# Kernel optimization log

Measured on AMD Instinct MI355X. Metric: run time of the kernel, lower is better.

The kernel has to match this reference:

```python
import jax, jax.numpy as jnp
import numpy as np

B, S, D = 2, 2048, 1024
H = 16
HD = D // H  # 64
SCALE = 1.0 / np.sqrt(HD).astype(np.float32)


def setup_inputs() -> dict:
    key = jax.random.key(0)
    ks = jax.random.split(key, 5)
    std = 0.02
    return {
        "x": jax.random.normal(ks[0], (B, S, D), dtype=jnp.float32),
        "W_qkv": jax.random.normal(ks[1], (D, 3 * D), dtype=jnp.float32) * std,
        "b_qkv": jnp.zeros((3 * D,), dtype=jnp.float32),
        "W_proj": jax.random.normal(ks[2], (D, D), dtype=jnp.float32) * std,
        "b_proj": jnp.zeros((D,), dtype=jnp.float32),
    }


def reference(x, W_qkv, b_qkv, W_proj, b_proj):
    bsz, seq_len, _ = x.shape
    qkv = x @ W_qkv + b_qkv  # [B,S,3D]
    qkv = qkv.reshape(bsz, seq_len, 3, H, HD)
    qkv = jnp.transpose(qkv, (2, 0, 3, 1, 4))  # [3,B,H,S,HD]
    q, k, v = qkv[0], qkv[1], qkv[2]
    scores = jnp.einsum("bhqd,bhkd->bhqk", q, k) * SCALE  # [B,H,S,S]
    causal = jnp.tril(jnp.ones((seq_len, seq_len), dtype=bool))
    scores = jnp.where(causal[None, None], scores, -jnp.inf)
    weights = jax.nn.softmax(scores, axis=-1)
    attn = jnp.einsum("bhqk,bhkd->bhqd", weights, v)  # [B,H,S,HD]
    attn = jnp.transpose(attn, (0, 2, 1, 3)).reshape(bsz, seq_len, H * HD)
    return attn @ W_proj + b_proj
```

## Files before the change

### kernel.cpp

```cpp
#include <hip/hip_runtime.h>
#include <stdint.h>

#define NB 2
#define NS 2048
#define ND 1024
#define NH 16
#define NHD 64
#define SCALE_QL2 0.1803368801111244f

typedef __attribute__((ext_vector_type(8))) short bf16x8;
typedef __attribute__((ext_vector_type(4))) float f32x4;
typedef __attribute__((ext_vector_type(16))) float f32x16;
typedef __attribute__((ext_vector_type(8))) unsigned short u16x8;

__device__ __forceinline__ unsigned short f2bf(float f) {
  union { float f; unsigned u; } v; v.f = f;
  unsigned r = v.u + 0x7FFFu + ((v.u >> 16) & 1u);
  return (unsigned short)(r >> 16);
}

__device__ __forceinline__ float bf2f(unsigned short u) {
  union { unsigned u; float f; } v; v.u = ((unsigned)u) << 16;
  return v.f;
}

__device__ __forceinline__ float fexp2(float x) { return __builtin_amdgcn_exp2f(x); }

__device__ __forceinline__ unsigned cvtpk(float a, float b) {
  unsigned r;
  asm("v_cvt_pk_bf16_f32 %0, %1, %2" : "=v"(r) : "v"(a), "v"(b));
  return r;
}

__device__ __forceinline__ void plswap(unsigned& a, unsigned& b) {
  asm("v_permlane32_swap_b32 %0, %1" : "+v"(a), "+v"(b));
}

__device__ __forceinline__ void gload16(const void* g, void* l) {
  __builtin_amdgcn_global_load_lds(
      (const __attribute__((address_space(1))) unsigned int*)g,
      (__attribute__((address_space(3))) unsigned int*)l, 16, 0, 0);
}


__global__ void cvt_x(const float* __restrict__ in, unsigned short* __restrict__ out) {
  int i = blockIdx.x * 256 + threadIdx.x;
  const float4* p = (const float4*)in + (size_t)i * 2;
  float4 a = p[0], b = p[1];
  u16x8 o;
  o[0] = f2bf(a.x); o[1] = f2bf(a.y); o[2] = f2bf(a.z); o[3] = f2bf(a.w);
  o[4] = f2bf(b.x); o[5] = f2bf(b.y); o[6] = f2bf(b.z); o[7] = f2bf(b.w);
  *((u16x8*)out + i) = o;
}

__global__ void transpose_cvt(const float* __restrict__ W, unsigned short* __restrict__ WT,
                              int rows, int cols) {
  __shared__ float tile[32][33];
  int bc = blockIdx.x * 32;
  int br = blockIdx.y * 32;
  int tx = threadIdx.x & 31, ty = threadIdx.x >> 5;
#pragma unroll
  for (int i = 0; i < 4; ++i)
    tile[ty + i * 8][tx] = W[(size_t)(br + ty + i * 8) * cols + bc + tx];
  __syncthreads();
#pragma unroll
  for (int i = 0; i < 4; ++i)
    WT[(size_t)(bc + ty + i * 8) * rows + br + tx] = f2bf(tile[tx][ty + i * 8]);
}

template <int EPI, int BN, int MINW>
__global__ __launch_bounds__(256, MINW) void gemm_bt(
    const unsigned short* __restrict__ A, const unsigned short* __restrict__ Bt,
    const float* __restrict__ bias, int NT,
    unsigned short* __restrict__ Oq, unsigned short* __restrict__ Ok,
    unsigned short* __restrict__ Ov, float* __restrict__ Of) {
  constexpr int WN = BN / 2;
  constexpr int NI = BN / 32;
  constexpr int RB = BN / 32;
  __shared__ __align__(16) unsigned short lA[128 * 64];
  __shared__ __align__(16) unsigned short lB[BN * 64];

  int bid = blockIdx.x;
  int cpx = gridDim.x >> 3;
  int swz = (bid & 7) * cpx + (bid >> 3);
  int mt = swz / NT, nt = swz % NT;
  int m0 = mt * 128, n0 = nt * BN;

  int t = threadIdx.x, lane = t & 63, w = t >> 6;
  int wm = w >> 1, wn = w & 1;

  f32x4 acc[4][NI] = {};

  const char* gA = (const char*)(A + (size_t)m0 * 1024);
  const char* gB = (const char*)(Bt + (size_t)n0 * 1024);

  for (int kt = 0; kt < 16; ++kt) {
    __syncthreads();
#pragma unroll
    for (int r = 0; r < 4; ++r) {
      int L = r * 4096 + t * 16;
      int row = L >> 7, cb = L & 127;
      int scb = cb ^ ((row & 7) << 4);
      gload16(gA + (size_t)row * 2048 + kt * 128 + scb, (char*)lA + (L - lane * 16));
    }
#pragma unroll
    for (int r = 0; r < RB; ++r) {
      int L = r * 4096 + t * 16;
      int row = L >> 7, cb = L & 127;
      int scb = cb ^ ((row & 7) << 4);
      gload16(gB + (size_t)row * 2048 + kt * 128 + scb, (char*)lB + (L - lane * 16));
    }
    __syncthreads();
#pragma unroll
    for (int kk = 0; kk < 2; ++kk) {
      bf16x8 af[4], bg[NI];
#pragma unroll
      for (int mi = 0; mi < 4; ++mi) {
        int row = wm * 64 + mi * 16 + (lane & 15);
        int byte = row * 128 + ((kk * 64 + (lane >> 4) * 16) ^ ((row & 7) << 4));
        af[mi] = *(const bf16x8*)((const char*)lA + byte);
      }
#pragma unroll
      for (int ni = 0; ni < NI; ++ni) {
        int row = wn * WN + ni * 16 + (lane & 15);
        int byte = row * 128 + ((kk * 64 + (lane >> 4) * 16) ^ ((row & 7) << 4));
        bg[ni] = *(const bf16x8*)((const char*)lB + byte);
      }
      __builtin_amdgcn_s_setprio(1);
#pragma unroll
      for (int mi = 0; mi < 4; ++mi)
#pragma unroll
        for (int ni = 0; ni < NI; ++ni)
          acc[mi][ni] = __builtin_amdgcn_mfma_f32_16x16x32_bf16(af[mi], bg[ni], acc[mi][ni], 0, 0, 0);
      __builtin_amdgcn_s_setprio(0);
    }
  }

#pragma unroll
  for (int mi = 0; mi < 4; ++mi)
#pragma unroll
    for (int ni = 0; ni < NI; ++ni) {
      int col = n0 + wn * WN + ni * 16 + (lane & 15);
      float bv = bias[col];
#pragma unroll
      for (int r = 0; r < 4; ++r) {
        int row = m0 + wm * 64 + mi * 16 + (lane >> 4) * 4 + r;
        float v = acc[mi][ni][r] + bv;
        if (EPI == 0) {
          int which = col >> 10, dd = col & 1023;
          int h = dd >> 6, hd = dd & 63;
          int b = row >> 11, s = row & 2047;
          size_t bh = (size_t)(b * 16 + h);
          if (which == 0)      Oq[(bh * 2048 + s) * 64 + hd] = f2bf(v * SCALE_QL2);
          else if (which == 1) Ok[(bh * 2048 + s) * 64 + hd] = f2bf(v);
          else                 Ov[(bh * 64 + hd) * 2048 + s] = f2bf(v);
        } else {
          Of[(size_t)row * 1024 + col] = v;
        }
      }
    }
}

__global__ __launch_bounds__(256, 4) void attn_split(
    const unsigned short* __restrict__ Qb, const unsigned short* __restrict__ Kb,
    const unsigned short* __restrict__ Vt,
    unsigned short* __restrict__ PO, float* __restrict__ PML) {
  __shared__ __align__(16) unsigned short lK[2][64 * 64];
  __shared__ __align__(16) unsigned short lV[2][64 * 64];

  int id = blockIdx.x;
  int bh = id & 31;
  int slot = 39 - (id >> 5);
  int a, g;
  if (slot < 4)       { a = 0; g = slot; }
  else if (slot < 12) { a = 1; g = slot - 4; }
  else if (slot < 24) { a = 2; g = slot - 12; }
  else                { a = 3; g = slot - 24; }
  int Tg = (a == 0) ? g : (a == 1) ? (g >> 1) : (a == 2) ? ((g * 11) >> 5) : (g >> 2);
  int T  = a * 4 + Tg;
  int c  = g - Tg * (a + 1);
  int t0 = c * 8;
  int tend = min(t0 + 7, 2 * T + 1);

  int t = threadIdx.x, lane = t & 63, w = t >> 6;
  int lo = lane & 31, hi = lane >> 5;
  int q0w = T * 128 + w * 32;
  int itmaxw = 2 * T + (w >> 1);
  int swzb = (lo & 7) << 4;

  const unsigned short* Qg = Qb + ((size_t)bh * 2048 + q0w + lo) * 64 + hi * 8;
  bf16x8 qf[4];
#pragma unroll
  for (int kk = 0; kk < 4; ++kk) qf[kk] = *(const bf16x8*)(Qg + kk * 16);

  f32x16 o0 = {}, o1 = {};
  float m = -1e30f, lsum = 0.f;

  const char* Kg = (const char*)(Kb + (size_t)bh * 2048 * 64);
  const char* Vg = (const char*)(Vt + (size_t)bh * 64 * 2048);

  int Lb = t * 16;
  auto STAGE = [&](int buf, int tile) {
    int s0 = tile * 64;
#pragma unroll
    for (int r = 0; r < 2; ++r) {
      int L = r * 4096 + Lb;
      int row = L >> 7, cb = L & 127;
      int scb = cb ^ ((row & 7) << 4);
      gload16(Kg + (size_t)(s0 + row) * 128 + scb, (char*)&lK[buf][0] + (L - lane * 16));
      gload16(Vg + (size_t)row * 4096 + (size_t)s0 * 2 + scb, (char*)&lV[buf][0] + (L - lane * 16));
    }
  };

  STAGE(0, t0);

  int cur = 0;
  for (int it = t0; it <= tend; ++it) {
    if (it < tend) {
      STAGE(cur ^ 1, it + 1);
      asm volatile("s_waitcnt vmcnt(4)" ::: "memory");
    } else {
      asm volatile("s_waitcnt vmcnt(0)" ::: "memory");
    }
    asm volatile("s_barrier" ::: "memory");

    if (it <= itmaxw) {
      const char* bK = (const char*)&lK[cur][0];
      const char* bV = (const char*)&lV[cur][0];

      f32x16 sv0 = {}, sv1 = {};
      __builtin_amdgcn_s_setprio(1);
#pragma unroll
      for (int kk = 0; kk < 4; ++kk) {
        int dby = 32 * kk + 16 * hi;
        bf16x8 k0 = *(const bf16x8*)(bK + lo * 128 + (dby ^ swzb));
        bf16x8 k1 = *(const bf16x8*)(bK + (32 + lo) * 128 + (dby ^ swzb));
        sv0 = __builtin_amdgcn_mfma_f32_32x32x16_bf16(k0, qf[kk], sv0, 0, 0, 0);
        sv1 = __builtin_amdgcn_mfma_f32_32x32x16_bf16(k1, qf[kk], sv1, 0, 0, 0);
      }
      __builtin_amdgcn_s_setprio(0);

      if (it == itmaxw) {
        int qg2 = q0w + lo, s0 = it * 64;
#pragma unroll
        for (int r = 0; r < 16; ++r) {
          int kv = s0 + (r & 3) + 8 * (r >> 2) + 4 * hi;
          if (kv > qg2) sv0[r] = -1e30f;
          if (kv + 32 > qg2) sv1[r] = -1e30f;
        }
      }

      float rmax = -1e30f;
#pragma unroll
      for (int r = 0; r < 16; ++r) rmax = fmaxf(rmax, fmaxf(sv0[r], sv1[r]));
      rmax = fmaxf(rmax, __shfl_xor(rmax, 32));

      if (__any(rmax > m + 8.0f)) {
        float mn = fmaxf(m, rmax);
        float sf = fexp2(m - mn);
        m = mn; lsum *= sf;
#pragma unroll
        for (int r = 0; r < 16; ++r) {
          float s = __shfl(sf, (r & 3) + 8 * (r >> 2) + 4 * hi);
          o0[r] *= s; o1[r] *= s;
        }
      }

      float rsum = 0.f;
#pragma unroll
      for (int r = 0; r < 16; ++r) {
        sv0[r] = fexp2(sv0[r] - m); rsum += sv0[r];
        sv1[r] = fexp2(sv1[r] - m); rsum += sv1[r];
      }
      rsum += __shfl_xor(rsum, 32);
      lsum += rsum;

      bf16x8 pa[4];
#pragma unroll
      for (int h2 = 0; h2 < 2; ++h2) {
        const f32x16& P = h2 ? sv1 : sv0;
#pragma unroll
        for (int kp = 0; kp < 2; ++kp) {
          unsigned a0 = cvtpk(P[8 * kp + 0], P[8 * kp + 1]);
          unsigned a1 = cvtpk(P[8 * kp + 2], P[8 * kp + 3]);
          unsigned b0 = cvtpk(P[8 * kp + 4], P[8 * kp + 5]);
          unsigned b1 = cvtpk(P[8 * kp + 6], P[8 * kp + 7]);
          plswap(a0, b0); plswap(a1, b1);
          union { unsigned u[4]; bf16x8 v; } uu;
          uu.u[0] = a0; uu.u[1] = a1; uu.u[2] = b0; uu.u[3] = b1;
          pa[2 * h2 + kp] = uu.v;
        }
      }

      __builtin_amdgcn_s_setprio(1);
#pragma unroll
      for (int dh = 0; dh < 2; ++dh) {
        f32x16& oc = dh ? o1 : o0;
#pragma unroll
        for (int ks = 0; ks < 4; ++ks) {
          int kvby = 32 * ks + 16 * hi;
          bf16x8 vf = *(const bf16x8*)(bV + (32 * dh + lo) * 128 + (kvby ^ swzb));
          oc = __builtin_amdgcn_mfma_f32_32x32x16_bf16(pa[ks], vf, oc, 0, 0, 0);
        }
      }
      __builtin_amdgcn_s_setprio(0);
    }

    asm volatile("s_barrier" ::: "memory");
    cur ^= 1;
  }

  size_t pobase = (size_t)(bh * 40 + slot) * 128;
#pragma unroll
  for (int r = 0; r < 16; ++r) {
    int crow = (r & 3) + 8 * (r >> 2) + 4 * hi;
    size_t rowoff = (pobase + w * 32 + crow) * 64 + lo;
    PO[rowoff]      = f2bf(o0[r]);
    PO[rowoff + 32] = f2bf(o1[r]);
  }
  if (hi == 0) {
    size_t mlbase = (size_t)(bh * 40 + slot) * 256 + w * 32 + lo;
    PML[mlbase]       = m;
    PML[mlbase + 128] = lsum;
  }
}

__global__ void attn_combine(const unsigned short* __restrict__ PO,
                             const float* __restrict__ PML,
                             unsigned short* __restrict__ attn) {
  int id = blockIdx.x * 256 + threadIdx.x;
  int dg = id & 7;
  int s  = (id >> 3) & 2047;
  int bh = id >> 14;
  int T = s >> 7, a = T >> 2;
  int nc = a + 1;
  int slot0 = (a + 1) * (T - 2 * a);
  int r128 = s & 127;
  int pb = bh * 40 + slot0;

  float mv[4], lv[4];
#pragma unroll
  for (int c = 0; c < 4; ++c) {
    if (c < nc) {
      mv[c] = PML[(size_t)(pb + c) * 256 + r128];
      lv[c] = PML[(size_t)(pb + c) * 256 + 128 + r128];
    } else { mv[c] = -1e30f; lv[c] = 0.f; }
  }
  float M = fmaxf(fmaxf(mv[0], mv[1]), fmaxf(mv[2], mv[3]));
  float wv[4], L = 0.f;
#pragma unroll
  for (int c = 0; c < 4; ++c) { wv[c] = fexp2(mv[c] - M); L += wv[c] * lv[c]; }
  float rcpL = 1.0f / L;

  float acc[8] = {};
#pragma unroll
  for (int c = 0; c < 4; ++c) {
    if (c < nc) {
      bf16x8 p = *(const bf16x8*)(PO + ((size_t)(pb + c) * 128 + r128) * 64 + dg * 8);
#pragma unroll
      for (int j = 0; j < 8; ++j) acc[j] += wv[c] * bf2f((unsigned short)p[j]);
    }
  }
  u16x8 o;
#pragma unroll
  for (int j = 0; j < 8; ++j) o[j] = f2bf(acc[j] * rcpL);
  int b = bh >> 4, h = bh & 15;
  *(u16x8*)(attn + ((size_t)(b * 2048 + s)) * 1024 + h * 64 + dg * 8) = o;
}

extern "C" void kernel_launch(void* const* d_in, const int* in_sizes, int n_in,
                              void* d_out, int out_size, void* d_ws, size_t ws_size,
                              hipStream_t stream) {
  const float* x      = (const float*)d_in[0];
  const float* W_qkv  = (const float*)d_in[1];
  const float* b_qkv  = (const float*)d_in[2];
  const float* W_proj = (const float*)d_in[3];
  const float* b_proj = (const float*)d_in[4];
  float* out = (float*)d_out;

  char* ws = (char*)d_ws;
  const size_t MB = 1u << 20;
  unsigned short* xb     = (unsigned short*)(ws);
  unsigned short* WqkvT  = (unsigned short*)(ws + 8 * MB);
  unsigned short* WprojT = (unsigned short*)(ws + 14 * MB);
  unsigned short* Qb     = (unsigned short*)(ws + 16 * MB);
  unsigned short* Kb     = (unsigned short*)(ws + 24 * MB);
  unsigned short* Vt     = (unsigned short*)(ws + 32 * MB);
  unsigned short* PO     = (unsigned short*)(ws + 40 * MB);
  float*          PML    = (float*)(ws + 60 * MB);
  unsigned short* attn   = xb;

  cvt_x<<<2048, 256, 0, stream>>>(x, xb);
  transpose_cvt<<<dim3(96, 32), 256, 0, stream>>>(W_qkv, WqkvT, 1024, 3072);
  transpose_cvt<<<dim3(32, 32), 256, 0, stream>>>(W_proj, WprojT, 1024, 1024);
  gemm_bt<0, 128, 2><<<768, 256, 0, stream>>>(xb, WqkvT, b_qkv, 24, Qb, Kb, Vt, nullptr);
  attn_split<<<1280, 256, 0, stream>>>(Qb, Kb, Vt, PO, PML);
  attn_combine<<<2048, 256, 0, stream>>>(PO, PML, attn);
  gemm_bt<1, 64, 5><<<512, 256, 0, stream>>>(attn, WprojT, b_proj, 16, nullptr, nullptr, nullptr, out);
}
```

Measured before the change: 121.1 us.

## Load K/V fragments directly from global memory, dropping LDS staging and barriers

Removes the double-buffered LDS staging of K and V tiles along with the block-wide barriers. Each wave now reads its MFMA operand fragments straight from global memory (relying on L1/L2 caching) and stops at its own causal limit. This eliminates LDS traffic and synchronization, but the four waves now fetch the same K/V data redundantly, and global-load latency is no longer hidden by prefetch.

```diff
diff --git a/kernel.cpp b/kernel.cpp
--- a/kernel.cpp
+++ b/kernel.cpp
@@ -165,9 +165,6 @@
     const unsigned short* __restrict__ Qb, const unsigned short* __restrict__ Kb,
     const unsigned short* __restrict__ Vt,
     unsigned short* __restrict__ PO, float* __restrict__ PML) {
-  __shared__ __align__(16) unsigned short lK[2][64 * 64];
-  __shared__ __align__(16) unsigned short lV[2][64 * 64];
-
   int id = blockIdx.x;
   int bh = id & 31;
   int slot = 39 - (id >> 5);
@@ -180,13 +177,12 @@
   int T  = a * 4 + Tg;
   int c  = g - Tg * (a + 1);
   int t0 = c * 8;
-  int tend = min(t0 + 7, 2 * T + 1);
 
   int t = threadIdx.x, lane = t & 63, w = t >> 6;
   int lo = lane & 31, hi = lane >> 5;
   int q0w = T * 128 + w * 32;
   int itmaxw = 2 * T + (w >> 1);
-  int swzb = (lo & 7) << 4;
+  int tendw = min(min(t0 + 7, 2 * T + 1), itmaxw);
 
   const unsigned short* Qg = Qb + ((size_t)bh * 2048 + q0w + lo) * 64 + hi * 8;
   bf16x8 qf[4];
@@ -196,118 +192,89 @@
   f32x16 o0 = {}, o1 = {};
   float m = -1e30f, lsum = 0.f;
 
-  const char* Kg = (const char*)(Kb + (size_t)bh * 2048 * 64);
-  const char* Vg = (const char*)(Vt + (size_t)bh * 64 * 2048);
-
-  int Lb = t * 16;
-  auto STAGE = [&](int buf, int tile) {
-    int s0 = tile * 64;
-#pragma unroll
-    for (int r = 0; r < 2; ++r) {
-      int L = r * 4096 + Lb;
-      int row = L >> 7, cb = L & 127;
-      int scb = cb ^ ((row & 7) << 4);
-      gload16(Kg + (size_t)(s0 + row) * 128 + scb, (char*)&lK[buf][0] + (L - lane * 16));
-      gload16(Vg + (size_t)row * 4096 + (size_t)s0 * 2 + scb, (char*)&lV[buf][0] + (L - lane * 16));
-    }
-  };
-
-  STAGE(0, t0);
-
-  int cur = 0;
-  for (int it = t0; it <= tend; ++it) {
-    if (it < tend) {
-      STAGE(cur ^ 1, it + 1);
-      asm volatile("s_waitcnt vmcnt(4)" ::: "memory");
-    } else {
-      asm volatile("s_waitcnt vmcnt(0)" ::: "memory");
-    }
-    asm volatile("s_barrier" ::: "memory");
-
-    if (it <= itmaxw) {
-      const char* bK = (const char*)&lK[cur][0];
-      const char* bV = (const char*)&lV[cur][0];
-
-      f32x16 sv0 = {}, sv1 = {};
-      __builtin_amdgcn_s_setprio(1);
-#pragma unroll
-      for (int kk = 0; kk < 4; ++kk) {
-        int dby = 32 * kk + 16 * hi;
-        bf16x8 k0 = *(const bf16x8*)(bK + lo * 128 + (dby ^ swzb));
-        bf16x8 k1 = *(const bf16x8*)(bK + (32 + lo) * 128 + (dby ^ swzb));
-        sv0 = __builtin_amdgcn_mfma_f32_32x32x16_bf16(k0, qf[kk], sv0, 0, 0, 0);
-        sv1 = __builtin_amdgcn_mfma_f32_32x32x16_bf16(k1, qf[kk], sv1, 0, 0, 0);
-      }
-      __builtin_amdgcn_s_setprio(0);
-
-      if (it == itmaxw) {
-        int qg2 = q0w + lo, s0 = it * 64;
-#pragma unroll
-        for (int r = 0; r < 16; ++r) {
-          int kv = s0 + (r & 3) + 8 * (r >> 2) + 4 * hi;
-          if (kv > qg2) sv0[r] = -1e30f;
-          if (kv + 32 > qg2) sv1[r] = -1e30f;
-        }
-      }
-
-      float rmax = -1e30f;
-#pragma unroll
-      for (int r = 0; r < 16; ++r) rmax = fmaxf(rmax, fmaxf(sv0[r], sv1[r]));
-      rmax = fmaxf(rmax, __shfl_xor(rmax, 32));
-
-      if (__any(rmax > m + 8.0f)) {
-        float mn = fmaxf(m, rmax);
-        float sf = fexp2(m - mn);
-        m = mn; lsum *= sf;
-#pragma unroll
-        for (int r = 0; r < 16; ++r) {
-          float s = __shfl(sf, (r & 3) + 8 * (r >> 2) + 4 * hi);
-          o0[r] *= s; o1[r] *= s;
-        }
-      }
-
-      float rsum = 0.f;
+  const char* Kg  = (const char*)(Kb + (size_t)bh * 2048 * 64);
+  const char* Vg  = (const char*)(Vt + (size_t)bh * 64 * 2048);
+  const char* Kr0 = Kg + lo * 128 + 16 * hi;
+  const char* Kr1 = Kg + (32 + lo) * 128 + 16 * hi;
+  const char* Vr  = Vg + lo * 4096 + 16 * hi;
+
+  for (int it = t0; it <= tendw; ++it) {
+    int s0 = it * 64;
+
+    f32x16 sv0 = {}, sv1 = {};
+    __builtin_amdgcn_s_setprio(1);
+#pragma unroll
+    for (int kk = 0; kk < 4; ++kk) {
+      bf16x8 k0 = *(const bf16x8*)(Kr0 + s0 * 128 + 32 * kk);
+      bf16x8 k1 = *(const bf16x8*)(Kr1 + s0 * 128 + 32 * kk);
+      sv0 = __builtin_amdgcn_mfma_f32_32x32x16_bf16(k0, qf[kk], sv0, 0, 0, 0);
+      sv1 = __builtin_amdgcn_mfma_f32_32x32x16_bf16(k1, qf[kk], sv1, 0, 0, 0);
+    }
+    __builtin_amdgcn_s_setprio(0);
+
+    if (it == itmaxw) {
+      int qg2 = q0w + lo;
 #pragma unroll
       for (int r = 0; r < 16; ++r) {
-        sv0[r] = fexp2(sv0[r] - m); rsum += sv0[r];
-        sv1[r] = fexp2(sv1[r] - m); rsum += sv1[r];
-      }
-      rsum += __shfl_xor(rsum, 32);
-      lsum += rsum;
-
-      bf16x8 pa[4];
-#pragma unroll
-      for (int h2 = 0; h2 < 2; ++h2) {
-        const f32x16& P = h2 ? sv1 : sv0;
-#pragma unroll
-        for (int kp = 0; kp < 2; ++kp) {
-          unsigned a0 = cvtpk(P[8 * kp + 0], P[8 * kp + 1]);
-          unsigned a1 = cvtpk(P[8 * kp + 2], P[8 * kp + 3]);
-          unsigned b0 = cvtpk(P[8 * kp + 4], P[8 * kp + 5]);
-          unsigned b1 = cvtpk(P[8 * kp + 6], P[8 * kp + 7]);
-          plswap(a0, b0); plswap(a1, b1);
-          union { unsigned u[4]; bf16x8 v; } uu;
-          uu.u[0] = a0; uu.u[1] = a1; uu.u[2] = b0; uu.u[3] = b1;
-          pa[2 * h2 + kp] = uu.v;
-        }
-      }
-
-      __builtin_amdgcn_s_setprio(1);
-#pragma unroll
-      for (int dh = 0; dh < 2; ++dh) {
-        f32x16& oc = dh ? o1 : o0;
-#pragma unroll
-        for (int ks = 0; ks < 4; ++ks) {
-          int kvby = 32 * ks + 16 * hi;
-          bf16x8 vf = *(const bf16x8*)(bV + (32 * dh + lo) * 128 + (kvby ^ swzb));
-          oc = __builtin_amdgcn_mfma_f32_32x32x16_bf16(pa[ks], vf, oc, 0, 0, 0);
-        }
-      }
-      __builtin_amdgcn_s_setprio(0);
-    }
-
-    asm volatile("s_barrier" ::: "memory");
-    cur ^= 1;
+        int kv = s0 + (r & 3) + 8 * (r >> 2) + 4 * hi;
+        if (kv > qg2) sv0[r] = -1e30f;
+        if (kv + 32 > qg2) sv1[r] = -1e30f;
+      }
+    }
+
+    float rmax = -1e30f;
+#pragma unroll
+    for (int r = 0; r < 16; ++r) rmax = fmaxf(rmax, fmaxf(sv0[r], sv1[r]));
+    rmax = fmaxf(rmax, __shfl_xor(rmax, 32));
+
+    if (__any(rmax > m + 8.0f)) {
+      float mn = fmaxf(m, rmax);
+      float sf = fexp2(m - mn);
+      m = mn; lsum *= sf;
+#pragma unroll
+      for (int r = 0; r < 16; ++r) {
+        float s = __shfl(sf, (r & 3) + 8 * (r >> 2) + 4 * hi);
+        o0[r] *= s; o1[r] *= s;
+      }
+    }
+
+    float rsum = 0.f;
+#pragma unroll
+    for (int r = 0; r < 16; ++r) {
+      sv0[r] = fexp2(sv0[r] - m); rsum += sv0[r];
+      sv1[r] = fexp2(sv1[r] - m); rsum += sv1[r];
+    }
+    rsum += __shfl_xor(rsum, 32);
+    lsum += rsum;
+
+    bf16x8 pa[4];
+#pragma unroll
+    for (int h2 = 0; h2 < 2; ++h2) {
+      const f32x16& P = h2 ? sv1 : sv0;
+#pragma unroll
+      for (int kp = 0; kp < 2; ++kp) {
+        unsigned a0 = cvtpk(P[8 * kp + 0], P[8 * kp + 1]);
+        unsigned a1 = cvtpk(P[8 * kp + 2], P[8 * kp + 3]);
+        unsigned b0 = cvtpk(P[8 * kp + 4], P[8 * kp + 5]);
+        unsigned b1 = cvtpk(P[8 * kp + 6], P[8 * kp + 7]);
+        plswap(a0, b0); plswap(a1, b1);
+        union { unsigned u[4]; bf16x8 v; } uu;
+        uu.u[0] = a0; uu.u[1] = a1; uu.u[2] = b0; uu.u[3] = b1;
+        pa[2 * h2 + kp] = uu.v;
+      }
+    }
+
+    __builtin_amdgcn_s_setprio(1);
+#pragma unroll
+    for (int dh = 0; dh < 2; ++dh) {
+      f32x16& oc = dh ? o1 : o0;
+#pragma unroll
+      for (int ks = 0; ks < 4; ++ks) {
+        bf16x8 vf = *(const bf16x8*)(Vr + dh * 131072 + s0 * 2 + 32 * ks);
+        oc = __builtin_amdgcn_mfma_f32_32x32x16_bf16(pa[ks], vf, oc, 0, 0, 0);
+      }
+    }
+    __builtin_amdgcn_s_setprio(0);
   }
 
   size_t pobase = (size_t)(bh * 40 + slot) * 128;
```

Result: slower. 162.4 us (+34.1%).
